# Optimization experiments

Hardware: AMD Instinct MI355X
Metric: run time of the kernel (lower is better)

## Reference

```python
import jax, jax.numpy as jnp
import numpy as np

EPS = 1e-10


def _make_spd(key, shape):
    # entrywise-nonnegative SPD: B>=0 -> B@B^T has nonnegative entries and is PSD;
    # + c*I keeps it well-conditioned and entrywise nonnegative.
    B = jax.random.uniform(key, shape, dtype=jnp.float32)
    D = jnp.einsum('...ij,...kj->...ik', B, B)
    return D + 0.05 * jnp.eye(3, dtype=jnp.float32)


def setup_inputs() -> dict:
    key = jax.random.key(0)
    k1, k2 = jax.random.split(key)
    shape = (2, 128, 128, 64, 3, 3)
    return {"D1": _make_spd(k1, shape), "D2": _make_spd(k2, shape)}


def _log_spd(D):
    # sanitize like torch.nan_to_num(..., nan=eps, posinf=eps, neginf=eps)
    D = jnp.nan_to_num(D, nan=EPS, posinf=EPS, neginf=EPS)
    D = jnp.abs(D)  # entrywise abs; input is symmetric so abs stays symmetric
    w, V = jnp.linalg.eigh(D)            # [...,3], [...,3,3]
    lw = jnp.log(w + EPS) + EPS
    # V @ diag(lw) @ V^T
    return jnp.einsum('...ij,...j,...kj->...ik', V, lw, V)


def reference(D1, D2):
    diff = _log_spd(D1) - _log_spd(D2)
    return jnp.mean(diff * diff)
```

## Files before the change

kernel.cpp:

```cpp
#include <hip/hip_runtime.h>
#include <math.h>

#define EPS_F 1e-10f

typedef __attribute__((ext_vector_type(2))) float f2;
typedef __attribute__((ext_vector_type(2))) unsigned int u2;

typedef const __attribute__((address_space(1))) char* gcp;
typedef __attribute__((address_space(3))) char* lcp;

__device__ __forceinline__ f2 v_fabs(f2 x) {
  u2 u = __builtin_bit_cast(u2, x);
  u &= 0x7fffffffu;
  return __builtin_bit_cast(f2, u);
}
__device__ __forceinline__ f2 v_max(f2 a, f2 b) { return __builtin_elementwise_max(a, b); }
__device__ __forceinline__ f2 v_min(f2 a, f2 b) { return __builtin_elementwise_min(a, b); }
__device__ __forceinline__ f2 v_log(f2 x) {
  f2 r; r.x = __logf(x.x); r.y = __logf(x.y); return r;
}
__device__ __forceinline__ f2 v_rcp(f2 x) {
  f2 r; r.x = __builtin_amdgcn_rcpf(x.x); r.y = __builtin_amdgcn_rcpf(x.y); return r;
}
__device__ __forceinline__ f2 v_rsq(f2 x) {
  f2 r; r.x = __builtin_amdgcn_rsqf(x.x); r.y = __builtin_amdgcn_rsqf(x.y); return r;
}
__device__ __forceinline__ f2 v_sqrt(f2 x) {
  f2 r; r.x = __builtin_amdgcn_sqrtf(x.x); r.y = __builtin_amdgcn_sqrtf(x.y); return r;
}
__device__ __forceinline__ f2 v_cos(f2 x) {
  f2 r; r.x = __cosf(x.x); r.y = __cosf(x.y); return r;
}

__device__ __forceinline__ f2 v_acos(f2 r) {
  const f2 t = v_fabs(r);
  const f2 s = v_sqrt(1.0f - t);
  f2 p = f2{-0.0012624911f, -0.0012624911f};
  p = p * t +  0.0066700901f;
  p = p * t + -0.0170881256f;
  p = p * t +  0.0308918810f;
  p = p * t + -0.0501743046f;
  p = p * t +  0.0889789874f;
  p = p * t + -0.2145988016f;
  p = p * t +  1.5707963050f;
  const f2 ac = s * p;
  f2 res;
  res.x = (r.x < 0.0f) ? (3.14159265358979f - ac.x) : ac.x;
  res.y = (r.y < 0.0f) ? (3.14159265358979f - ac.y) : ac.y;
  return res;
}

__device__ __forceinline__ float pair_loss(f2 a00, f2 a01, f2 a02,
                                           f2 a11, f2 a12, f2 a22) {
  a00 = v_fabs(a00); a01 = v_fabs(a01); a02 = v_fabs(a02);
  a11 = v_fabs(a11); a12 = v_fabs(a12); a22 = v_fabs(a22);

  const f2 q   = (a00 + a11 + a22) * (1.0f / 3.0f);
  const f2 b00 = a00 - q, b11 = a11 - q, b22 = a22 - q;
  const f2 p2  = b00 * b00 + b11 * b11 + b22 * b22 +
                 2.0f * (a01 * a01 + a02 * a02 + a12 * a12);

  const f2 p2c  = v_max(p2 * (1.0f / 6.0f), 1e-10f * q * q + 1e-35f);
  const f2 pinv = v_rsq(p2c);
  const f2 p    = p2c * pinv;

  const f2 detB = b00 * (b11 * b22 - a12 * a12)
                - a01 * (a01 * b22 - a12 * a02)
                + a02 * (a01 * a12 - b11 * a02);
  f2 r = detB * 0.5f * pinv * pinv * pinv;
  r = v_min(f2{1.0f, 1.0f}, v_max(f2{-1.0f, -1.0f}, r));
  const f2 phi  = v_acos(r) * (1.0f / 3.0f);
  const f2 twop = 2.0f * p;
  const f2 l1 = q + twop * v_cos(phi);
  const f2 l3 = q + twop * v_cos(phi + 2.0943951023931953f);
  const f2 l2 = 3.0f * q - l1 - l3;

  const f2 s00 = a00 * a00 + a01 * a01 + a02 * a02;
  const f2 s01 = a00 * a01 + a01 * a11 + a02 * a12;
  const f2 s02 = a00 * a02 + a01 * a12 + a02 * a22;
  const f2 s11 = a01 * a01 + a11 * a11 + a12 * a12;
  const f2 s12 = a01 * a02 + a11 * a12 + a12 * a22;
  const f2 s22 = a02 * a02 + a12 * a12 + a22 * a22;

  const f2 g12 = l1 - l2, g23 = l2 - l3;
  f2 alpha, gamma;
  alpha.x = (g12.x >= g23.x) ? l1.x : l3.x;  gamma.x = (g12.x >= g23.x) ? l3.x : l1.x;
  alpha.y = (g12.y >= g23.y) ? l1.y : l3.y;  gamma.y = (g12.y >= g23.y) ? l3.y : l1.y;
  const f2 beta = l2;

  const f2 f_a = v_log(alpha + EPS_F);
  const f2 f_b = v_log(beta  + EPS_F);
  const f2 f_g = v_log(gamma + EPS_F);

  const f2 inv_den_a = v_rcp((alpha - beta) * (alpha - gamma));

  const f2 gap = gamma - beta;
  const f2 ga  = gamma - alpha;
  const f2 agap = v_fabs(gap);
  const f2 thr  = 1e-5f * v_max(v_fabs(beta), v_fabs(gamma));
  const f2 mid  = 0.5f * (beta + gamma) + EPS_F;
  f2 num, den;
  num.x = (agap.x > thr.x) ? (f_g.x - f_b.x) : 1.0f;
  den.x = (agap.x > thr.x) ? (gap.x * ga.x) : (mid.x * ga.x);
  num.y = (agap.y > thr.y) ? (f_g.y - f_b.y) : 1.0f;
  den.y = (agap.y > thr.y) ? (gap.y * ga.y) : (mid.y * ga.y);
  const f2 cg = num * v_rcp(den);
  const f2 wd = (f_a - f_b) * inv_den_a;

  const f2 sbg = beta + gamma, pbg = beta * gamma;
  const f2 sab = alpha + beta, pab = alpha * beta;
  const f2 c2 = wd + cg;
  const f2 c1 = -(wd * sbg + cg * sab);
  const f2 c0 = f_b + wd * pbg + cg * pab;

  const f2 L0 = c2 * s00 + c1 * a00 + c0;
  const f2 L1 = c2 * s01 + c1 * a01;
  const f2 L2 = c2 * s02 + c1 * a02;
  const f2 L3 = c2 * s11 + c1 * a11 + c0;
  const f2 L4 = c2 * s12 + c1 * a12;
  const f2 L5 = c2 * s22 + c1 * a22 + c0;

  const float d0 = L0.x - L0.y;
  const float d1 = L1.x - L1.y;
  const float d2 = L2.x - L2.y;
  const float d3 = L3.x - L3.y;
  const float d4 = L4.x - L4.y;
  const float d5 = L5.x - L5.y;
  return d0 * d0 + d3 * d3 + d5 * d5 + 2.0f * (d1 * d1 + d2 * d2 + d4 * d4);
}

#define WAVE_BYTES 4608
#define T_BYTES    2304

__global__ void __launch_bounds__(256, 8)
leloss_partial(const float* __restrict__ d1, const float* __restrict__ d2,
               float* __restrict__ partial, int nmat) {
  __shared__ float lds[4 * WAVE_BYTES / 4];

  const int tid  = threadIdx.x;
  const int lane = tid & 63;
  const int wid  = tid >> 6;
  const int wgid = blockIdx.x * 4 + wid;
  const int p0   = wgid * 64;

  float acc = 0.0f;

  if (p0 + 64 <= nmat) {
    const char* s1 = reinterpret_cast<const char*>(d1) + (size_t)p0 * 36;
    const char* s2 = reinterpret_cast<const char*>(d2) + (size_t)p0 * 36;
    char* lbase = reinterpret_cast<char*>(lds) + wid * WAVE_BYTES;

#pragma unroll
    for (int j = 0; j < 4; ++j) {
      const int o = j * 1024 + lane * 16;
      const char* src = (o < T_BYTES) ? (s1 + o) : (s2 + (o - T_BYTES));
      __builtin_amdgcn_global_load_lds((gcp)src, (lcp)(lbase + o), 16, 0, 0);
    }
#pragma unroll
    for (int j = 0; j < 2; ++j) {
      const int o = 4096 + j * 256 + lane * 4;
      const char* src = s2 + (o - T_BYTES);
      __builtin_amdgcn_global_load_lds((gcp)src, (lcp)(lbase + o), 4, 0, 0);
    }
    asm volatile("s_waitcnt vmcnt(0)" ::: "memory");

    const float* m1 = lds + wid * (WAVE_BYTES / 4) + lane * 9;
    const float* m2 = m1 + (T_BYTES / 4);
    const f2 a00 = f2{m1[0], m2[0]};
    const f2 a01 = f2{m1[1], m2[1]};
    const f2 a02 = f2{m1[2], m2[2]};
    const f2 a11 = f2{m1[4], m2[4]};
    const f2 a12 = f2{m1[5], m2[5]};
    const f2 a22 = f2{m1[8], m2[8]};
    acc = pair_loss(a00, a01, a02, a11, a12, a22);
  } else {
    const int pr = p0 + lane;
    if (pr < nmat) {
      const size_t base = (size_t)pr * 9;
      const f2 a00 = f2{d1[base + 0], d2[base + 0]};
      const f2 a01 = f2{d1[base + 1], d2[base + 1]};
      const f2 a02 = f2{d1[base + 2], d2[base + 2]};
      const f2 a11 = f2{d1[base + 4], d2[base + 4]};
      const f2 a12 = f2{d1[base + 5], d2[base + 5]};
      const f2 a22 = f2{d1[base + 8], d2[base + 8]};
      acc = pair_loss(a00, a01, a02, a11, a12, a22);
    }
  }

#pragma unroll
  for (int off = 32; off > 0; off >>= 1) acc += __shfl_down(acc, off, 64);

  __shared__ float wsum[4];
  if ((tid & 63) == 0) wsum[wid] = acc;
  __syncthreads();
  if (tid == 0) {
    partial[blockIdx.x] = wsum[0] + wsum[1] + wsum[2] + wsum[3];
  }
}

__global__ void __launch_bounds__(256)
leloss_reduce(const float* __restrict__ partial, int n,
              float* __restrict__ out, double inv_count) {
  double s = 0.0;
  for (int i = threadIdx.x; i < n; i += 256) s += (double)partial[i];
#pragma unroll
  for (int off = 32; off > 0; off >>= 1) s += __shfl_down(s, off, 64);

  __shared__ double wsum[4];
  const int lane = threadIdx.x & 63;
  const int wid  = threadIdx.x >> 6;
  if (lane == 0) wsum[wid] = s;
  __syncthreads();
  if (threadIdx.x == 0) {
    const double total = wsum[0] + wsum[1] + wsum[2] + wsum[3];
    out[0] = (float)(total * inv_count);
  }
}

extern "C" void kernel_launch(void* const* d_in, const int* in_sizes, int n_in,
                              void* d_out, int out_size, void* d_ws, size_t ws_size,
                              hipStream_t stream) {
  const float* d1 = (const float*)d_in[0];
  const float* d2 = (const float*)d_in[1];
  float* out = (float*)d_out;
  float* partial = (float*)d_ws;

  const long long nelem = (long long)in_sizes[0];
  const int nmat = (int)(nelem / 9);
  const int nblocks = (nmat + 255) / 256;

  leloss_partial<<<nblocks, 256, 0, stream>>>(d1, d2, partial, nmat);

  const double inv_count = 1.0 / ((double)nmat * 9.0);
  leloss_reduce<<<1, 256, 0, stream>>>(partial, nblocks, out, inv_count);
}
```

Before: 38.80 us.

## Process two 64-matrix slices per wave with overlapped async LDS loads

Each wave now handles 128 matrices in two slices. It issues the global-to-LDS loads for both slices up front, then waits only for the first slice (vmcnt(6)) and computes it while the second slice is still in flight. The block count is halved and the per-block LDS footprint doubles, with launch bounds lowered to 4 waves per EU. The aim is to hide memory latency behind the eigen/log math, at the cost of fewer resident waves and fewer blocks for a small problem (about 2M matrices).

```diff
diff --git a/kernel.cpp b/kernel.cpp
--- a/kernel.cpp
+++ b/kernel.cpp
@@ -129,61 +129,91 @@
   return d0 * d0 + d3 * d3 + d5 * d5 + 2.0f * (d1 * d1 + d2 * d2 + d4 * d4);
 }
 
-#define WAVE_BYTES 4608
-#define T_BYTES    2304
-
-__global__ void __launch_bounds__(256, 8)
+#define CH_T_BYTES 2304
+#define CH_BYTES   4608
+#define SLICES_PER_WAVE 2
+#define WAVE_LDS (CH_BYTES * SLICES_PER_WAVE)
+#define BLOCK_LDS (WAVE_LDS * 4)
+
+__global__ void __launch_bounds__(256, 4)
 leloss_partial(const float* __restrict__ d1, const float* __restrict__ d2,
                float* __restrict__ partial, int nmat) {
-  __shared__ float lds[4 * WAVE_BYTES / 4];
+  __shared__ float lds[BLOCK_LDS / 4];
 
   const int tid  = threadIdx.x;
   const int lane = tid & 63;
   const int wid  = tid >> 6;
   const int wgid = blockIdx.x * 4 + wid;
-  const int p0   = wgid * 64;
+  const int p0   = wgid * 128;
+  const int p1   = p0 + 64;
+
+  char* lb0 = reinterpret_cast<char*>(lds) + wid * WAVE_LDS;
+  char* lb1 = lb0 + CH_BYTES;
 
   float acc = 0.0f;
 
-  if (p0 + 64 <= nmat) {
-    const char* s1 = reinterpret_cast<const char*>(d1) + (size_t)p0 * 36;
-    const char* s2 = reinterpret_cast<const char*>(d2) + (size_t)p0 * 36;
-    char* lbase = reinterpret_cast<char*>(lds) + wid * WAVE_BYTES;
-
-#pragma unroll
-    for (int j = 0; j < 4; ++j) {
-      const int o = j * 1024 + lane * 16;
-      const char* src = (o < T_BYTES) ? (s1 + o) : (s2 + (o - T_BYTES));
-      __builtin_amdgcn_global_load_lds((gcp)src, (lcp)(lbase + o), 16, 0, 0);
-    }
-#pragma unroll
-    for (int j = 0; j < 2; ++j) {
-      const int o = 4096 + j * 256 + lane * 4;
-      const char* src = s2 + (o - T_BYTES);
-      __builtin_amdgcn_global_load_lds((gcp)src, (lcp)(lbase + o), 4, 0, 0);
-    }
+  if (p1 + 64 <= nmat) {
+    const char* base1 = reinterpret_cast<const char*>(d1);
+    const char* base2 = reinterpret_cast<const char*>(d2);
+
+#pragma unroll
+    for (int s = 0; s < 2; ++s) {
+      const size_t gb = (size_t)(s == 0 ? p0 : p1) * 36;
+      char* lb = (s == 0) ? lb0 : lb1;
+#pragma unroll
+      for (int j = 0; j < 4; ++j) {
+        const int o = j * 1024 + lane * 16;
+        const char* src = (o < CH_T_BYTES) ? (base1 + gb + o)
+                                           : (base2 + gb + (o - CH_T_BYTES));
+        __builtin_amdgcn_global_load_lds((gcp)src, (lcp)(lb + o), 16, 0, 0);
+      }
+#pragma unroll
+      for (int j = 0; j < 2; ++j) {
+        const int o = 4096 + j * 256 + lane * 4;
+        __builtin_amdgcn_global_load_lds((gcp)(base2 + gb + (o - CH_T_BYTES)),
+                                         (lcp)(lb + o), 4, 0, 0);
+      }
+    }
+
+    asm volatile("s_waitcnt vmcnt(6)" ::: "memory");
+    {
+      const float* m1 = reinterpret_cast<const float*>(lb0) + lane * 9;
+      const float* m2 = reinterpret_cast<const float*>(lb0 + CH_T_BYTES) + lane * 9;
+      const f2 a00 = f2{m1[0], m2[0]};
+      const f2 a01 = f2{m1[1], m2[1]};
+      const f2 a02 = f2{m1[2], m2[2]};
+      const f2 a11 = f2{m1[4], m2[4]};
+      const f2 a12 = f2{m1[5], m2[5]};
+      const f2 a22 = f2{m1[8], m2[8]};
+      acc = pair_loss(a00, a01, a02, a11, a12, a22);
+    }
+
     asm volatile("s_waitcnt vmcnt(0)" ::: "memory");
-
-    const float* m1 = lds + wid * (WAVE_BYTES / 4) + lane * 9;
-    const float* m2 = m1 + (T_BYTES / 4);
-    const f2 a00 = f2{m1[0], m2[0]};
-    const f2 a01 = f2{m1[1], m2[1]};
-    const f2 a02 = f2{m1[2], m2[2]};
-    const f2 a11 = f2{m1[4], m2[4]};
-    const f2 a12 = f2{m1[5], m2[5]};
-    const f2 a22 = f2{m1[8], m2[8]};
-    acc = pair_loss(a00, a01, a02, a11, a12, a22);
+    {
+      const float* m1 = reinterpret_cast<const float*>(lb1) + lane * 9;
+      const float* m2 = reinterpret_cast<const float*>(lb1 + CH_T_BYTES) + lane * 9;
+      const f2 a00 = f2{m1[0], m2[0]};
+      const f2 a01 = f2{m1[1], m2[1]};
+      const f2 a02 = f2{m1[2], m2[2]};
+      const f2 a11 = f2{m1[4], m2[4]};
+      const f2 a12 = f2{m1[5], m2[5]};
+      const f2 a22 = f2{m1[8], m2[8]};
+      acc += pair_loss(a00, a01, a02, a11, a12, a22);
+    }
   } else {
-    const int pr = p0 + lane;
-    if (pr < nmat) {
-      const size_t base = (size_t)pr * 9;
-      const f2 a00 = f2{d1[base + 0], d2[base + 0]};
-      const f2 a01 = f2{d1[base + 1], d2[base + 1]};
-      const f2 a02 = f2{d1[base + 2], d2[base + 2]};
-      const f2 a11 = f2{d1[base + 4], d2[base + 4]};
-      const f2 a12 = f2{d1[base + 5], d2[base + 5]};
-      const f2 a22 = f2{d1[base + 8], d2[base + 8]};
-      acc = pair_loss(a00, a01, a02, a11, a12, a22);
+#pragma unroll
+    for (int s = 0; s < 2; ++s) {
+      const int pr = (s == 0 ? p0 : p1) + lane;
+      if (pr < nmat) {
+        const size_t base = (size_t)pr * 9;
+        const f2 a00 = f2{d1[base + 0], d2[base + 0]};
+        const f2 a01 = f2{d1[base + 1], d2[base + 1]};
+        const f2 a02 = f2{d1[base + 2], d2[base + 2]};
+        const f2 a11 = f2{d1[base + 4], d2[base + 4]};
+        const f2 a12 = f2{d1[base + 5], d2[base + 5]};
+        const f2 a22 = f2{d1[base + 8], d2[base + 8]};
+        acc += pair_loss(a00, a01, a02, a11, a12, a22);
+      }
     }
   }
 
@@ -191,7 +221,7 @@
   for (int off = 32; off > 0; off >>= 1) acc += __shfl_down(acc, off, 64);
 
   __shared__ float wsum[4];
-  if ((tid & 63) == 0) wsum[wid] = acc;
+  if (lane == 0) wsum[wid] = acc;
   __syncthreads();
   if (tid == 0) {
     partial[blockIdx.x] = wsum[0] + wsum[1] + wsum[2] + wsum[3];
@@ -227,7 +257,7 @@
 
   const long long nelem = (long long)in_sizes[0];
   const int nmat = (int)(nelem / 9);
-  const int nblocks = (nmat + 255) / 256;
+  const int nblocks = (nmat + 511) / 512;
 
   leloss_partial<<<nblocks, 256, 0, stream>>>(d1, d2, partial, nmat);
 
```

New measurement: 34.25 us. 11.7% less time.
